# Performance work log

Measured on AMD Instinct MI355X. Metric: run time of the kernel, lower is better.

## Reference

```python
import math
import jax, jax.numpy as jnp
import numpy as np


def _expmap0(u):
    # geoopt Lorentz (k=1) expmap0 followed by projection back onto the hyperboloid.
    # Minkowski norm of the tangent input (geoopt clamps at 1e-8 before sqrt).
    u0 = u[..., :1]
    us = u[..., 1:]
    mink = -u0 * u0 + jnp.sum(us * us, axis=-1, keepdims=True)
    nomin = jnp.sqrt(jnp.maximum(mink, 1e-8))
    r = jnp.sinh(nomin) * u / nomin
    space = r[..., 1:]
    time = jnp.sqrt(1.0 + jnp.sum(space * space, axis=-1, keepdims=True))  # project()
    return jnp.concatenate([time, space], axis=-1)


def setup_inputs() -> dict:
    key = jax.random.key(0)
    B, T, E, H = 2, 1024, 1024, 16
    ks = jax.random.split(key, 8)
    s = 0.02
    return {
        "x": jax.random.normal(ks[0], (B, T, E), jnp.float32),
        "Wqkv": jax.random.normal(ks[1], (3 * E, E), jnp.float32) * s,
        "bqkv": jnp.zeros((3 * E,), jnp.float32),
        "Wout": jax.random.normal(ks[2], (E, E), jnp.float32) * s,
        "bout": jnp.zeros((E,), jnp.float32),
        "Wimp": jax.random.normal(ks[3], (1, E), jnp.float32) * s,
        "bimp": jnp.zeros((1,), jnp.float32),
        "Walpha": jax.random.normal(ks[4], (H, E), jnp.float32) * s,
        "balpha": jnp.zeros((H,), jnp.float32),
        "spike_threshold": jnp.asarray(0.5, jnp.float32),
        "log_k": jnp.full((H,), 0.54, jnp.float32),
        "qk_scale": jnp.asarray(0.1, jnp.float32),
    }


def reference(x, Wqkv, bqkv, Wout, bout, Wimp, bimp, Walpha, balpha,
              spike_threshold, log_k, qk_scale):
    B, T, C = x.shape
    H = log_k.shape[0]
    D = C // H

    importance = jax.nn.sigmoid(x @ Wimp.T + bimp)          # (B,T,1)
    # torch.tril on the (T,1) trailing dims keeps every element -> no-op mask.
    spikes = (importance > spike_threshold).astype(x.dtype)
    spike_mask = spikes.reshape(B, 1, T, 1)

    alpha = jax.nn.sigmoid(x @ Walpha.T + balpha)           # (B,T,H)
    alpha = jnp.transpose(alpha, (0, 2, 1))[..., None]      # (B,H,T,1)

    qkv = (x @ Wqkv.T + bqkv).reshape(B, T, 3, H, D)
    q = jnp.transpose(qkv[:, :, 0], (0, 2, 1, 3))           # (B,H,T,D)
    k = jnp.transpose(qkv[:, :, 1], (0, 2, 1, 3))
    v = jnp.transpose(qkv[:, :, 2], (0, 2, 1, 3))

    scores_euclid = jnp.einsum('bhtd,bhsd->bhts', q, k) / math.sqrt(D)

    safe_scale = jax.nn.sigmoid(qk_scale) * 1.5
    qn = q / jnp.maximum(jnp.linalg.norm(q, axis=-1, keepdims=True), 1e-12) * safe_scale
    kn = k / jnp.maximum(jnp.linalg.norm(k, axis=-1, keepdims=True), 1e-12) * safe_scale
    q_hyp = _expmap0(qn)
    k_hyp = _expmap0(kn)

    inner = (-jnp.einsum('bhti,bhsi->bhts', q_hyp[..., :1], k_hyp[..., :1])
             + jnp.einsum('bhtd,bhsd->bhts', q_hyp[..., 1:], k_hyp[..., 1:]))
    curv_k = (jax.nn.softplus(log_k) + 1e-6).reshape(1, H, 1, 1)
    mdot = jnp.maximum(-inner, 1.0 + 1e-6)
    dist = jnp.arccosh(mdot)
    scores_hyper = -(dist * dist) / curv_k

    scores = (1.0 - alpha) * scores_euclid + alpha * scores_hyper
    causal = jnp.tril(jnp.ones((T, T), bool))
    scores = jnp.where(causal[None, None], scores, -jnp.inf)

    attn = jax.nn.softmax(scores, axis=-1) * spike_mask     # dropout disabled (eval)
    y = jnp.einsum('bhts,bhsd->bhtd', attn, v)
    y = jnp.transpose(y, (0, 2, 1, 3)).reshape(B, T, C)
    return y @ Wout.T + bout
```

## Files before the change

### kernel.cpp

```cpp
#include <hip/hip_runtime.h>
#include <math.h>

#define B_ 2
#define T_ 1024
#define E_ 1024
#define H_ 16
#define D_ 64
#define M_ (B_*T_)

typedef __bf16 bf16x8 __attribute__((ext_vector_type(8)));
typedef __bf16 bf16x4 __attribute__((ext_vector_type(4)));
typedef float f32x4 __attribute__((ext_vector_type(4)));

__device__ __forceinline__ void* ldsp(__bf16* base, int row, int byte) {
  return (char*)base + row * 128 + (byte ^ ((row & 7) << 4));
}

__device__ __forceinline__ void gload_lds16(const void* g, void* l) {
  __builtin_amdgcn_global_load_lds((const __attribute__((address_space(1))) void*)g,
                                   (__attribute__((address_space(3))) void*)l, 16, 0, 0);
}

#define XV4 524288
#define WQV4 786432
#define WOV4 262144
#define TOTV4 (XV4 + WQV4 + WOV4)
__global__ __launch_bounds__(256) void conv_kernel(
    const float* __restrict__ x, const float* __restrict__ Wqkv,
    const float* __restrict__ Wout,
    __bf16* __restrict__ xb, __bf16* __restrict__ Wqkvb, __bf16* __restrict__ Woutb) {
  for (size_t i = (size_t)blockIdx.x * blockDim.x + threadIdx.x; i < TOTV4;
       i += (size_t)gridDim.x * blockDim.x) {
    const float4* src; __bf16* dst; size_t off;
    if (i < XV4)            { src = (const float4*)x;    dst = xb;    off = i; }
    else if (i < XV4+WQV4)  { src = (const float4*)Wqkv; dst = Wqkvb; off = i - XV4; }
    else                    { src = (const float4*)Wout; dst = Woutb; off = i - XV4 - WQV4; }
    float4 val = src[off];
    bf16x4 o = {(__bf16)val.x, (__bf16)val.y, (__bf16)val.z, (__bf16)val.w};
    *(bf16x4*)(dst + off * 4) = o;
  }
}

__global__ __launch_bounds__(256) void imp_alpha_kernel(
    const float* __restrict__ x,
    const float* __restrict__ Wimp, const float* __restrict__ bimp,
    const float* __restrict__ Walpha, const float* __restrict__ balpha,
    const float* __restrict__ thr_p,
    float* __restrict__ spike, float* __restrict__ alpha) {
  int m = blockIdx.x;
  int tid = threadIdx.x;
  const float* xr = x + (size_t)m * E_;
  float part[17];
#pragma unroll
  for (int i = 0; i < 17; ++i) part[i] = 0.f;
  for (int e = tid; e < E_; e += 256) {
    float xv = xr[e];
    part[16] += xv * Wimp[e];
#pragma unroll
    for (int h = 0; h < 16; ++h) part[h] += xv * Walpha[h * E_ + e];
  }
  __shared__ float red[17][4];
  int lane = tid & 63, wv = tid >> 6;
#pragma unroll
  for (int i = 0; i < 17; ++i) {
    float v = part[i];
    for (int off = 32; off > 0; off >>= 1) v += __shfl_down(v, off, 64);
    if (lane == 0) red[i][wv] = v;
  }
  __syncthreads();
  if (tid < 17) {
    float v = red[tid][0] + red[tid][1] + red[tid][2] + red[tid][3];
    if (tid == 16) {
      float z = v + bimp[0];
      float sig = 1.f / (1.f + expf(-z));
      spike[m] = (sig > thr_p[0]) ? 1.f : 0.f;
    } else {
      float z = v + balpha[tid];
      float a = 1.f / (1.f + expf(-z));
      int b = m >> 10, t = m & (T_ - 1);
      alpha[((size_t)(b * H_ + tid)) * T_ + t] = a;
    }
  }
}

__global__ __launch_bounds__(256) void qkv_gemm_kernel(
    const __bf16* __restrict__ A, const __bf16* __restrict__ Bm,
    const float* __restrict__ bias,
    __bf16* __restrict__ q, __bf16* __restrict__ k, __bf16* __restrict__ v) {
  __shared__ __bf16 As[128 * 32];
  __shared__ __bf16 Bs[128 * 32];
  const int K = E_;
  int tid = threadIdx.x;
  int w = tid >> 6, lane = tid & 63, lr = lane & 15, g = lane >> 4;
  int m0 = blockIdx.y * 128, n0 = blockIdx.x * 128;
  int wr = (w >> 1) * 64, wc = (w & 1) * 64;

  int task0 = tid, task1 = tid + 256;
  int r0s = task0 >> 2, c0s = task0 & 3;
  int r1s = task1 >> 2, c1s = task1 & 3;
  const __bf16* gA0 = A + (size_t)(m0 + r0s) * K + c0s * 8;
  const __bf16* gA1 = A + (size_t)(m0 + r1s) * K + c1s * 8;
  const __bf16* gB0 = Bm + (size_t)(n0 + r0s) * K + c0s * 8;
  const __bf16* gB1 = Bm + (size_t)(n0 + r1s) * K + c1s * 8;
  __bf16* lA0 = As + task0 * 8;
  __bf16* lA1 = As + task1 * 8;
  __bf16* lB0 = Bs + task0 * 8;
  __bf16* lB1 = Bs + task1 * 8;

  f32x4 acc[4][4];
#pragma unroll
  for (int i = 0; i < 4; ++i)
#pragma unroll
    for (int j = 0; j < 4; ++j) acc[i][j] = (f32x4){0.f, 0.f, 0.f, 0.f};

  for (int k0 = 0; k0 < K; k0 += 32) {
    gload_lds16(gA0, lA0); gload_lds16(gA1, lA1);
    gload_lds16(gB0, lB0); gload_lds16(gB1, lB1);
    gA0 += 32; gA1 += 32; gB0 += 32; gB1 += 32;
    __syncthreads();
    bf16x8 af[4], bf[4];
#pragma unroll
    for (int i = 0; i < 4; ++i) af[i] = *(bf16x8*)&As[(wr + i * 16 + lr) * 32 + g * 8];
#pragma unroll
    for (int j = 0; j < 4; ++j) bf[j] = *(bf16x8*)&Bs[(wc + j * 16 + lr) * 32 + g * 8];
#pragma unroll
    for (int i = 0; i < 4; ++i)
#pragma unroll
      for (int j = 0; j < 4; ++j)
        acc[i][j] = __builtin_amdgcn_mfma_f32_16x16x32_bf16(af[i], bf[j], acc[i][j], 0, 0, 0);
    __syncthreads();
  }

#pragma unroll
  for (int i = 0; i < 4; ++i) {
#pragma unroll
    for (int r = 0; r < 4; ++r) {
      int m = m0 + wr + i * 16 + g * 4 + r;
      int b = m >> 10, t = m & (T_ - 1);
#pragma unroll
      for (int j = 0; j < 4; ++j) {
        int n = n0 + wc + j * 16 + lr;
        float val = acc[i][j][r] + bias[n];
        int comp = n >> 10, h = (n >> 6) & 15, d = n & 63;
        __bf16* dst = (comp == 0) ? q : ((comp == 1) ? k : v);
        dst[(((size_t)(b * H_ + h)) * T_ + t) * 64 + d] = (__bf16)val;
      }
    }
  }
}

__global__ __launch_bounds__(256) void hyp_kernel(
    const __bf16* __restrict__ q, const __bf16* __restrict__ k,
    const float* __restrict__ qk_scale_p,
    __bf16* __restrict__ qh, __bf16* __restrict__ khn) {
  int wid = blockIdx.x * 4 + (threadIdx.x >> 6);
  int lane = threadIdx.x & 63;
  int is_k = wid >> 15;
  int row = wid & 32767;
  const __bf16* src = (is_k ? k : q) + (size_t)row * 64;
  float u = (float)src[lane];
  float nsq = u * u;
#pragma unroll
  for (int off = 32; off > 0; off >>= 1) nsq += __shfl_xor(nsq, off, 64);
  float norm = fmaxf(sqrtf(nsq), 1e-12f);
  float ss = 1.5f / (1.f + expf(-qk_scale_p[0]));
  float un = u / norm * ss;
  float s2 = un * un;
  float tot = s2;
#pragma unroll
  for (int off = 32; off > 0; off >>= 1) tot += __shfl_xor(tot, off, 64);
  float un0 = __shfl(un, 0, 64);
  float mink = tot - 2.f * un0 * un0;
  float nomin = sqrtf(fmaxf(mink, 1e-8f));
  float sc = sinhf(nomin) / nomin;
  float r = sc * un;
  float sp2 = (lane == 0) ? 0.f : r * r;
  float sps = sp2;
#pragma unroll
  for (int off = 32; off > 0; off >>= 1) sps += __shfl_xor(sps, off, 64);
  float tm = sqrtf(1.f + sps);
  float outv = (lane == 0) ? tm : r;
  if (is_k && lane != 0) outv = -outv;
  (is_k ? khn : qh)[(size_t)row * 64 + lane] = (__bf16)outv;
}

__global__ __launch_bounds__(256) void attn_kernel(
    const __bf16* __restrict__ q, const __bf16* __restrict__ k, const __bf16* __restrict__ v,
    const __bf16* __restrict__ qh, const __bf16* __restrict__ khn,
    const float* __restrict__ alpha, const float* __restrict__ spike,
    const float* __restrict__ log_k, __bf16* __restrict__ y) {
  __shared__ __bf16 q_s[64 * 64];
  __shared__ __bf16 qh_s[64 * 64];
  __shared__ __bf16 k_s[64 * 64];
  __shared__ __bf16 kh_s[64 * 64];
  __shared__ __bf16 vt_s[64 * 64];
  __shared__ __bf16 p_s[64 * 64];

  int bid = blockIdx.x;
  int bq = bid >> 5;
  int qi = (bq < 8) ? (15 - bq) : (bq - 8);
  int bh = bid & 31;
  int b = bh >> 4, h = bh & 15;
  int t0 = qi * 64;
  int tid = threadIdx.x;
  int w = tid >> 6, lane = tid & 63;
  int lr = lane & 15, g = lane >> 4;
  int trow = w * 16;
  const size_t base = (size_t)bh * T_ * 64;

#pragma unroll
  for (int it = 0; it < 2; ++it) {
    int task = tid + it * 256;
    int row = task >> 3, cj = task & 7;
    bf16x8 a = *(const bf16x8*)(q + base + (size_t)(t0 + row) * 64 + cj * 8);
    bf16x8 c = *(const bf16x8*)(qh + base + (size_t)(t0 + row) * 64 + cj * 8);
    *(bf16x8*)ldsp(q_s, row, cj * 16) = a;
    *(bf16x8*)ldsp(qh_s, row, cj * 16) = c;
  }

  float curv = log1pf(expf(log_k[h])) + 1e-6f;
  float hc = 0.69314718056f / curv;
  const float ec = 0.18033688f;
  int tg[4];
  float al[4], spv[4];
#pragma unroll
  for (int r = 0; r < 4; ++r) {
    tg[r] = t0 + trow + g * 4 + r;
    al[r] = alpha[(size_t)bh * T_ + tg[r]];
    spv[r] = spike[(size_t)b * T_ + tg[r]];
  }

  __syncthreads();
  bf16x8 aq0 = *(bf16x8*)ldsp(q_s, trow + lr, g * 16);
  bf16x8 aq1 = *(bf16x8*)ldsp(q_s, trow + lr, 64 + g * 16);
  bf16x8 ah0 = *(bf16x8*)ldsp(qh_s, trow + lr, g * 16);
  bf16x8 ah1 = *(bf16x8*)ldsp(qh_s, trow + lr, 64 + g * 16);

  float m_r[4] = {-1e30f, -1e30f, -1e30f, -1e30f};
  float l_r[4] = {0.f, 0.f, 0.f, 0.f};
  f32x4 acc[4];
#pragma unroll
  for (int n = 0; n < 4; ++n) acc[n] = (f32x4){0.f, 0.f, 0.f, 0.f};

  for (int st = 0; st <= qi; ++st) {
    int s0 = st * 64;
    bool diag = (st == qi);
    __syncthreads();
#pragma unroll
    for (int it = 0; it < 2; ++it) {
      int task = tid + it * 256;
      int row = task >> 3, cj = task & 7;
      bf16x8 a = *(const bf16x8*)(k + base + (size_t)(s0 + row) * 64 + cj * 8);
      bf16x8 c = *(const bf16x8*)(khn + base + (size_t)(s0 + row) * 64 + cj * 8);
      *(bf16x8*)ldsp(k_s, row, cj * 16) = a;
      *(bf16x8*)ldsp(kh_s, row, cj * 16) = c;
    }
#pragma unroll
    for (int it = 0; it < 2; ++it) {
      int task = tid + it * 256;
      int srow = task & 63, dc = task >> 6;
      bf16x8 a = *(const bf16x8*)(v + base + (size_t)(s0 + srow) * 64 + dc * 8);
#pragma unroll
      for (int i = 0; i < 8; ++i)
        *(__bf16*)ldsp(vt_s, dc * 8 + i, srow * 2) = a[i];
    }
    __syncthreads();

    float pv[4][4];
    float pmax[4] = {-1e30f, -1e30f, -1e30f, -1e30f};
#pragma unroll
    for (int j = 0; j < 4; ++j) {
      if (diag && (s0 + j * 16 > t0 + trow + 15)) {
#pragma unroll
        for (int r = 0; r < 4; ++r) pv[j][r] = -1e30f;
        continue;
      }
      bf16x8 bk0 = *(bf16x8*)ldsp(k_s, j * 16 + lr, g * 16);
      bf16x8 bk1 = *(bf16x8*)ldsp(k_s, j * 16 + lr, 64 + g * 16);
      f32x4 z = {0.f, 0.f, 0.f, 0.f};
      z = __builtin_amdgcn_mfma_f32_16x16x32_bf16(aq0, bk0, z, 0, 0, 0);
      f32x4 se = __builtin_amdgcn_mfma_f32_16x16x32_bf16(aq1, bk1, z, 0, 0, 0);
      bf16x8 bh0 = *(bf16x8*)ldsp(kh_s, j * 16 + lr, g * 16);
      bf16x8 bh1 = *(bf16x8*)ldsp(kh_s, j * 16 + lr, 64 + g * 16);
      f32x4 z2 = {0.f, 0.f, 0.f, 0.f};
      z2 = __builtin_amdgcn_mfma_f32_16x16x32_bf16(ah0, bh0, z2, 0, 0, 0);
      f32x4 sh = __builtin_amdgcn_mfma_f32_16x16x32_bf16(ah1, bh1, z2, 0, 0, 0);
      int sg = s0 + j * 16 + lr;
#pragma unroll
      for (int r = 0; r < 4; ++r) {
        float sc_e = se[r] * ec;
        float md = fmaxf(sh[r], 1.0f + 1e-6f);
        float l2 = __log2f(md + sqrtf(fmaf(md, md, -1.f)));
        float t = fmaf(l2 * l2, hc, sc_e);
        float s = fmaf(-al[r], t, sc_e);
        if (diag && sg > tg[r]) s = -1e30f;
        pv[j][r] = s;
        pmax[r] = fmaxf(pmax[r], s);
      }
    }
#pragma unroll
    for (int r = 0; r < 4; ++r) {
      float mx = pmax[r];
      mx = fmaxf(mx, __shfl_xor(mx, 1, 64));
      mx = fmaxf(mx, __shfl_xor(mx, 2, 64));
      mx = fmaxf(mx, __shfl_xor(mx, 4, 64));
      mx = fmaxf(mx, __shfl_xor(mx, 8, 64));
      float mn = fmaxf(m_r[r], mx);
      float fac = exp2f(m_r[r] - mn);
      m_r[r] = mn;
      float ls = 0.f;
#pragma unroll
      for (int j = 0; j < 4; ++j) { pv[j][r] = exp2f(pv[j][r] - mn); ls += pv[j][r]; }
      ls += __shfl_xor(ls, 1, 64);
      ls += __shfl_xor(ls, 2, 64);
      ls += __shfl_xor(ls, 4, 64);
      ls += __shfl_xor(ls, 8, 64);
      l_r[r] = l_r[r] * fac + ls;
#pragma unroll
      for (int n = 0; n < 4; ++n) acc[n][r] *= fac;
    }
#pragma unroll
    for (int j = 0; j < 4; ++j)
#pragma unroll
      for (int r = 0; r < 4; ++r)
        *(__bf16*)ldsp(p_s, trow + g * 4 + r, (j * 16 + lr) * 2) = (__bf16)pv[j][r];
    __syncthreads();

    bf16x8 ap0 = *(bf16x8*)ldsp(p_s, trow + lr, g * 16);
    bf16x8 ap1 = *(bf16x8*)ldsp(p_s, trow + lr, 64 + g * 16);
#pragma unroll
    for (int n = 0; n < 4; ++n) {
      bf16x8 bv0 = *(bf16x8*)ldsp(vt_s, n * 16 + lr, g * 16);
      bf16x8 bv1 = *(bf16x8*)ldsp(vt_s, n * 16 + lr, 64 + g * 16);
      acc[n] = __builtin_amdgcn_mfma_f32_16x16x32_bf16(ap0, bv0, acc[n], 0, 0, 0);
      acc[n] = __builtin_amdgcn_mfma_f32_16x16x32_bf16(ap1, bv1, acc[n], 0, 0, 0);
    }
  }

#pragma unroll
  for (int r = 0; r < 4; ++r) {
    float iv = spv[r] / l_r[r];
#pragma unroll
    for (int n = 0; n < 4; ++n) {
      y[((size_t)(b * T_ + tg[r])) * E_ + h * 64 + n * 16 + lr] =
          (__bf16)(acc[n][r] * iv);
    }
  }
}

__global__ __launch_bounds__(256) void out_gemm_kernel(
    const __bf16* __restrict__ A, const __bf16* __restrict__ Bm,
    const float* __restrict__ bias, float* __restrict__ outp) {
  __shared__ __bf16 As[128 * 32];
  __shared__ __bf16 Bs[128 * 32];
  const int K = E_;
  int tid = threadIdx.x;
  int w = tid >> 6, lane = tid & 63, lr = lane & 15, g = lane >> 4;
  int m0 = blockIdx.y * 128, n0 = blockIdx.x * 128;
  int wr = (w >> 1) * 64, wc = (w & 1) * 64;

  int task0 = tid, task1 = tid + 256;
  int r0s = task0 >> 2, c0s = task0 & 3;
  int r1s = task1 >> 2, c1s = task1 & 3;
  const __bf16* gA0 = A + (size_t)(m0 + r0s) * K + c0s * 8;
  const __bf16* gA1 = A + (size_t)(m0 + r1s) * K + c1s * 8;
  const __bf16* gB0 = Bm + (size_t)(n0 + r0s) * K + c0s * 8;
  const __bf16* gB1 = Bm + (size_t)(n0 + r1s) * K + c1s * 8;
  __bf16* lA0 = As + task0 * 8;
  __bf16* lA1 = As + task1 * 8;
  __bf16* lB0 = Bs + task0 * 8;
  __bf16* lB1 = Bs + task1 * 8;

  f32x4 acc[4][4];
#pragma unroll
  for (int i = 0; i < 4; ++i)
#pragma unroll
    for (int j = 0; j < 4; ++j) acc[i][j] = (f32x4){0.f, 0.f, 0.f, 0.f};

  for (int k0 = 0; k0 < K; k0 += 32) {
    gload_lds16(gA0, lA0); gload_lds16(gA1, lA1);
    gload_lds16(gB0, lB0); gload_lds16(gB1, lB1);
    gA0 += 32; gA1 += 32; gB0 += 32; gB1 += 32;
    __syncthreads();
    bf16x8 af[4], bf[4];
#pragma unroll
    for (int i = 0; i < 4; ++i) af[i] = *(bf16x8*)&As[(wr + i * 16 + lr) * 32 + g * 8];
#pragma unroll
    for (int j = 0; j < 4; ++j) bf[j] = *(bf16x8*)&Bs[(wc + j * 16 + lr) * 32 + g * 8];
#pragma unroll
    for (int i = 0; i < 4; ++i)
#pragma unroll
      for (int j = 0; j < 4; ++j)
        acc[i][j] = __builtin_amdgcn_mfma_f32_16x16x32_bf16(af[i], bf[j], acc[i][j], 0, 0, 0);
    __syncthreads();
  }

#pragma unroll
  for (int i = 0; i < 4; ++i) {
#pragma unroll
    for (int r = 0; r < 4; ++r) {
      int m = m0 + wr + i * 16 + g * 4 + r;
#pragma unroll
      for (int j = 0; j < 4; ++j) {
        int n = n0 + wc + j * 16 + lr;
        outp[(size_t)m * E_ + n] = acc[i][j][r] + bias[n];
      }
    }
  }
}

extern "C" void kernel_launch(void* const* d_in, const int* in_sizes, int n_in,
                              void* d_out, int out_size, void* d_ws, size_t ws_size,
                              hipStream_t stream) {
  const float* x      = (const float*)d_in[0];
  const float* Wqkv   = (const float*)d_in[1];
  const float* bqkv   = (const float*)d_in[2];
  const float* Wout   = (const float*)d_in[3];
  const float* bout   = (const float*)d_in[4];
  const float* Wimp   = (const float*)d_in[5];
  const float* bimp   = (const float*)d_in[6];
  const float* Walpha = (const float*)d_in[7];
  const float* balpha = (const float*)d_in[8];
  const float* thr    = (const float*)d_in[9];
  const float* log_k  = (const float*)d_in[10];
  const float* qk_sc  = (const float*)d_in[11];
  float* out = (float*)d_out;

  char* ws = (char*)d_ws;
  size_t off = 0;
  auto alloc = [&](size_t bytes) -> void* {
    void* p = (void*)(ws + off);
    off += (bytes + 255) & ~(size_t)255;
    return p;
  };
  const size_t qkv_elems = (size_t)B_ * H_ * T_ * D_;
  __bf16* xb    = (__bf16*)alloc((size_t)M_ * E_ * 2);
  __bf16* Wqkvb = (__bf16*)alloc((size_t)3 * E_ * E_ * 2);
  __bf16* Woutb = (__bf16*)alloc((size_t)E_ * E_ * 2);
  __bf16* q   = (__bf16*)alloc(qkv_elems * 2);
  __bf16* k   = (__bf16*)alloc(qkv_elems * 2);
  __bf16* v   = (__bf16*)alloc(qkv_elems * 2);
  __bf16* qh  = (__bf16*)alloc(qkv_elems * 2);
  __bf16* khn = (__bf16*)alloc(qkv_elems * 2);
  __bf16* yw  = (__bf16*)alloc((size_t)M_ * E_ * 2);
  float* alphaw = (float*)alloc((size_t)B_ * H_ * T_ * sizeof(float));
  float* spikew = (float*)alloc((size_t)M_ * sizeof(float));

  conv_kernel<<<1024, 256, 0, stream>>>(x, Wqkv, Wout, xb, Wqkvb, Woutb);
  imp_alpha_kernel<<<M_, 256, 0, stream>>>(x, Wimp, bimp, Walpha, balpha, thr,
                                           spikew, alphaw);
  qkv_gemm_kernel<<<dim3(24, 16), 256, 0, stream>>>(xb, Wqkvb, bqkv, q, k, v);
  hyp_kernel<<<(2 * B_ * H_ * T_) / 4, 256, 0, stream>>>(q, k, qk_sc, qh, khn);
  attn_kernel<<<B_ * H_ * (T_ / 64), 256, 0, stream>>>(q, k, v, qh, khn,
                                                       alphaw, spikew, log_k, yw);
  out_gemm_kernel<<<dim3(8, 16), 256, 0, stream>>>(yw, Woutb, bout, out);
}
```

Baseline: 157.9 us.

## Split attention into per-wave query tiles with split-KV partials and merge

Attention now gives each wave its own 16-row query tile and processes alternate key tiles (two halves), writing unnormalised partial accumulators plus running max and sum. A new merge kernel combines the two halves and applies the spike mask and normalisation. V is pre-transposed once by a new kernel so PV operands load straight from global memory, and block-wide LDS staging and barriers are dropped. The aim is better load balance and more parallelism under the causal mask, and less synchronisation. The cost is that K, KH and V are no longer shared through LDS across waves, so L2 traffic rises, and the two extra launches add partial-buffer traffic.

```diff
diff --git a/kernel.cpp b/kernel.cpp
--- a/kernel.cpp
+++ b/kernel.cpp
@@ -184,57 +184,69 @@
   (is_k ? khn : qh)[(size_t)row * 64 + lane] = (__bf16)outv;
 }
 
-__global__ __launch_bounds__(256) void attn_kernel(
-    const __bf16* __restrict__ q, const __bf16* __restrict__ k, const __bf16* __restrict__ v,
-    const __bf16* __restrict__ qh, const __bf16* __restrict__ khn,
-    const float* __restrict__ alpha, const float* __restrict__ spike,
-    const float* __restrict__ log_k, __bf16* __restrict__ y) {
-  __shared__ __bf16 q_s[64 * 64];
-  __shared__ __bf16 qh_s[64 * 64];
-  __shared__ __bf16 k_s[64 * 64];
-  __shared__ __bf16 kh_s[64 * 64];
-  __shared__ __bf16 vt_s[64 * 64];
-  __shared__ __bf16 p_s[64 * 64];
-
-  int bid = blockIdx.x;
-  int bq = bid >> 5;
-  int qi = (bq < 8) ? (15 - bq) : (bq - 8);
-  int bh = bid & 31;
-  int b = bh >> 4, h = bh & 15;
-  int t0 = qi * 64;
-  int tid = threadIdx.x;
-  int w = tid >> 6, lane = tid & 63;
-  int lr = lane & 15, g = lane >> 4;
-  int trow = w * 16;
-  const size_t base = (size_t)bh * T_ * 64;
-
+__global__ __launch_bounds__(256) void vtr_kernel(
+    const __bf16* __restrict__ v, __bf16* __restrict__ vt) {
+  __shared__ __bf16 tile[64][65];
+  int bh = blockIdx.x >> 4;
+  int s0 = (blockIdx.x & 15) * 64;
+  int tid = threadIdx.x;
 #pragma unroll
   for (int it = 0; it < 2; ++it) {
     int task = tid + it * 256;
-    int row = task >> 3, cj = task & 7;
-    bf16x8 a = *(const bf16x8*)(q + base + (size_t)(t0 + row) * 64 + cj * 8);
-    bf16x8 c = *(const bf16x8*)(qh + base + (size_t)(t0 + row) * 64 + cj * 8);
-    *(bf16x8*)ldsp(q_s, row, cj * 16) = a;
-    *(bf16x8*)ldsp(qh_s, row, cj * 16) = c;
-  }
+    int r = task >> 3, c = (task & 7) * 8;
+    bf16x8 a = *(const bf16x8*)(v + ((size_t)bh * T_ + s0 + r) * 64 + c);
+#pragma unroll
+    for (int i = 0; i < 8; ++i) tile[r][c + i] = a[i];
+  }
+  __syncthreads();
+#pragma unroll
+  for (int it = 0; it < 2; ++it) {
+    int task = tid + it * 256;
+    int dd = task >> 3, sc = (task & 7) * 8;
+    bf16x8 o;
+#pragma unroll
+    for (int i = 0; i < 8; ++i) o[i] = tile[sc + i][dd];
+    *(bf16x8*)(vt + ((size_t)bh * 64 + dd) * T_ + s0 + sc) = o;
+  }
+}
+
+__global__ __launch_bounds__(256) void attn_kernel(
+    const __bf16* __restrict__ q, const __bf16* __restrict__ k,
+    const __bf16* __restrict__ qh, const __bf16* __restrict__ khn,
+    const __bf16* __restrict__ vt,
+    const float* __restrict__ alpha, const float* __restrict__ log_k,
+    __bf16* __restrict__ pacc, float* __restrict__ pml) {
+  __shared__ __bf16 pslab_all[4][16 * 64];
+  int tid = threadIdx.x;
+  int w = tid >> 6, lane = tid & 63;
+  int wid = blockIdx.x * 4 + w;
+  int bh = wid & 31;
+  int rest = wid >> 5;
+  int half = rest & 1;
+  int qt = rest >> 1;
+  int h = bh & 15;
+  int lr = lane & 15, g = lane >> 4;
+  int n_st = (qt >> 2) + 1;
+  const size_t base = (size_t)bh * T_ * 64;
+  const size_t vtb = (size_t)bh * 64 * T_;
+  __bf16* pslab = pslab_all[w];
+
+  const __bf16* qrow = q + base + (size_t)(qt * 16 + lr) * 64;
+  const __bf16* qhrow = qh + base + (size_t)(qt * 16 + lr) * 64;
+  bf16x8 aq0 = *(const bf16x8*)(qrow + g * 8);
+  bf16x8 aq1 = *(const bf16x8*)(qrow + 32 + g * 8);
+  bf16x8 ah0 = *(const bf16x8*)(qhrow + g * 8);
+  bf16x8 ah1 = *(const bf16x8*)(qhrow + 32 + g * 8);
 
   float curv = log1pf(expf(log_k[h])) + 1e-6f;
   float hc = 0.69314718056f / curv;
   const float ec = 0.18033688f;
-  int tg[4];
-  float al[4], spv[4];
+  int tg[4]; float al[4];
 #pragma unroll
   for (int r = 0; r < 4; ++r) {
-    tg[r] = t0 + trow + g * 4 + r;
+    tg[r] = qt * 16 + g * 4 + r;
     al[r] = alpha[(size_t)bh * T_ + tg[r]];
-    spv[r] = spike[(size_t)b * T_ + tg[r]];
-  }
-
-  __syncthreads();
-  bf16x8 aq0 = *(bf16x8*)ldsp(q_s, trow + lr, g * 16);
-  bf16x8 aq1 = *(bf16x8*)ldsp(q_s, trow + lr, 64 + g * 16);
-  bf16x8 ah0 = *(bf16x8*)ldsp(qh_s, trow + lr, g * 16);
-  bf16x8 ah1 = *(bf16x8*)ldsp(qh_s, trow + lr, 64 + g * 16);
+  }
 
   float m_r[4] = {-1e30f, -1e30f, -1e30f, -1e30f};
   float l_r[4] = {0.f, 0.f, 0.f, 0.f};
@@ -242,46 +254,27 @@
 #pragma unroll
   for (int n = 0; n < 4; ++n) acc[n] = (f32x4){0.f, 0.f, 0.f, 0.f};
 
-  for (int st = 0; st <= qi; ++st) {
+  for (int st = half; st < n_st; st += 2) {
     int s0 = st * 64;
-    bool diag = (st == qi);
-    __syncthreads();
-#pragma unroll
-    for (int it = 0; it < 2; ++it) {
-      int task = tid + it * 256;
-      int row = task >> 3, cj = task & 7;
-      bf16x8 a = *(const bf16x8*)(k + base + (size_t)(s0 + row) * 64 + cj * 8);
-      bf16x8 c = *(const bf16x8*)(khn + base + (size_t)(s0 + row) * 64 + cj * 8);
-      *(bf16x8*)ldsp(k_s, row, cj * 16) = a;
-      *(bf16x8*)ldsp(kh_s, row, cj * 16) = c;
-    }
-#pragma unroll
-    for (int it = 0; it < 2; ++it) {
-      int task = tid + it * 256;
-      int srow = task & 63, dc = task >> 6;
-      bf16x8 a = *(const bf16x8*)(v + base + (size_t)(s0 + srow) * 64 + dc * 8);
-#pragma unroll
-      for (int i = 0; i < 8; ++i)
-        *(__bf16*)ldsp(vt_s, dc * 8 + i, srow * 2) = a[i];
-    }
-    __syncthreads();
-
+    bool diag = (st == n_st - 1);
     float pv[4][4];
     float pmax[4] = {-1e30f, -1e30f, -1e30f, -1e30f};
 #pragma unroll
     for (int j = 0; j < 4; ++j) {
-      if (diag && (s0 + j * 16 > t0 + trow + 15)) {
+      if (diag && (s0 + j * 16 > qt * 16 + 15)) {
 #pragma unroll
         for (int r = 0; r < 4; ++r) pv[j][r] = -1e30f;
         continue;
       }
-      bf16x8 bk0 = *(bf16x8*)ldsp(k_s, j * 16 + lr, g * 16);
-      bf16x8 bk1 = *(bf16x8*)ldsp(k_s, j * 16 + lr, 64 + g * 16);
+      const __bf16* kr = k + base + (size_t)(s0 + j * 16 + lr) * 64;
+      const __bf16* khr = khn + base + (size_t)(s0 + j * 16 + lr) * 64;
+      bf16x8 bk0 = *(const bf16x8*)(kr + g * 8);
+      bf16x8 bk1 = *(const bf16x8*)(kr + 32 + g * 8);
       f32x4 z = {0.f, 0.f, 0.f, 0.f};
       z = __builtin_amdgcn_mfma_f32_16x16x32_bf16(aq0, bk0, z, 0, 0, 0);
       f32x4 se = __builtin_amdgcn_mfma_f32_16x16x32_bf16(aq1, bk1, z, 0, 0, 0);
-      bf16x8 bh0 = *(bf16x8*)ldsp(kh_s, j * 16 + lr, g * 16);
-      bf16x8 bh1 = *(bf16x8*)ldsp(kh_s, j * 16 + lr, 64 + g * 16);
+      bf16x8 bh0 = *(const bf16x8*)(khr + g * 8);
+      bf16x8 bh1 = *(const bf16x8*)(khr + 32 + g * 8);
       f32x4 z2 = {0.f, 0.f, 0.f, 0.f};
       z2 = __builtin_amdgcn_mfma_f32_16x16x32_bf16(ah0, bh0, z2, 0, 0, 0);
       f32x4 sh = __builtin_amdgcn_mfma_f32_16x16x32_bf16(ah1, bh1, z2, 0, 0, 0);
@@ -323,28 +316,60 @@
     for (int j = 0; j < 4; ++j)
 #pragma unroll
       for (int r = 0; r < 4; ++r)
-        *(__bf16*)ldsp(p_s, trow + g * 4 + r, (j * 16 + lr) * 2) = (__bf16)pv[j][r];
-    __syncthreads();
-
-    bf16x8 ap0 = *(bf16x8*)ldsp(p_s, trow + lr, g * 16);
-    bf16x8 ap1 = *(bf16x8*)ldsp(p_s, trow + lr, 64 + g * 16);
+        *(__bf16*)ldsp(pslab, g * 4 + r, (j * 16 + lr) * 2) = (__bf16)pv[j][r];
+    bf16x8 ap0 = *(bf16x8*)ldsp(pslab, lr, g * 16);
+    bf16x8 ap1 = *(bf16x8*)ldsp(pslab, lr, 64 + g * 16);
 #pragma unroll
     for (int n = 0; n < 4; ++n) {
-      bf16x8 bv0 = *(bf16x8*)ldsp(vt_s, n * 16 + lr, g * 16);
-      bf16x8 bv1 = *(bf16x8*)ldsp(vt_s, n * 16 + lr, 64 + g * 16);
+      const __bf16* vr = vt + vtb + (size_t)(n * 16 + lr) * T_ + s0;
+      bf16x8 bv0 = *(const bf16x8*)(vr + g * 8);
+      bf16x8 bv1 = *(const bf16x8*)(vr + 32 + g * 8);
       acc[n] = __builtin_amdgcn_mfma_f32_16x16x32_bf16(ap0, bv0, acc[n], 0, 0, 0);
       acc[n] = __builtin_amdgcn_mfma_f32_16x16x32_bf16(ap1, bv1, acc[n], 0, 0, 0);
     }
   }
 
-#pragma unroll
-  for (int r = 0; r < 4; ++r) {
-    float iv = spv[r] / l_r[r];
-#pragma unroll
-    for (int n = 0; n < 4; ++n) {
-      y[((size_t)(b * T_ + tg[r])) * E_ + h * 64 + n * 16 + lr] =
-          (__bf16)(acc[n][r] * iv);
-    }
+  int pidx = ((bh << 6) + qt) * 2 + half;
+  __bf16* pa = pacc + (size_t)pidx * 1024;
+#pragma unroll
+  for (int n = 0; n < 4; ++n)
+#pragma unroll
+    for (int r = 0; r < 4; ++r)
+      pa[(g * 4 + r) * 64 + n * 16 + lr] = (__bf16)acc[n][r];
+  if (lr == 0) {
+#pragma unroll
+    for (int r = 0; r < 4; ++r) {
+      pml[(size_t)pidx * 32 + g * 4 + r] = m_r[r];
+      pml[(size_t)pidx * 32 + 16 + g * 4 + r] = l_r[r];
+    }
+  }
+}
+
+__global__ __launch_bounds__(256) void merge_kernel(
+    const __bf16* __restrict__ pacc, const float* __restrict__ pml,
+    const float* __restrict__ spike, __bf16* __restrict__ yw) {
+  int tid = threadIdx.x;
+  int w = tid >> 6, lane = tid & 63;
+  int wid = blockIdx.x * 4 + w;
+  int bh = wid & 31;
+  int qt = wid >> 5;
+  int b = bh >> 4, h = bh & 15;
+  size_t i1 = ((size_t)(bh << 6) + qt) * 2;
+  size_t i2 = i1 + 1;
+  const __bf16* a1 = pacc + i1 * 1024;
+  const __bf16* a2 = pacc + i2 * 1024;
+#pragma unroll 4
+  for (int row = 0; row < 16; ++row) {
+    float m1 = pml[i1 * 32 + row], l1 = pml[i1 * 32 + 16 + row];
+    float m2 = pml[i2 * 32 + row], l2 = pml[i2 * 32 + 16 + row];
+    float mm = fmaxf(m1, m2);
+    float f1 = exp2f(m1 - mm), f2 = exp2f(m2 - mm);
+    float l = l1 * f1 + l2 * f2;
+    int t = qt * 16 + row;
+    float iv = spike[(size_t)b * T_ + t] / l;
+    float val = ((float)a1[row * 64 + lane] * f1 +
+                 (float)a2[row * 64 + lane] * f2) * iv;
+    yw[(size_t)(b * T_ + t) * E_ + h * 64 + lane] = (__bf16)val;
   }
 }
 
@@ -442,16 +467,21 @@
   __bf16* v   = (__bf16*)alloc(qkv_elems * 2);
   __bf16* qh  = (__bf16*)alloc(qkv_elems * 2);
   __bf16* khn = (__bf16*)alloc(qkv_elems * 2);
+  __bf16* vt  = (__bf16*)alloc(qkv_elems * 2);
   __bf16* yw  = (__bf16*)alloc((size_t)M_ * E_ * 2);
   float* alphaw = (float*)alloc((size_t)B_ * H_ * T_ * sizeof(float));
   float* spikew = (float*)alloc((size_t)M_ * sizeof(float));
+  float* pml    = (float*)alloc((size_t)4096 * 32 * sizeof(float));
+  __bf16* pacc = (__bf16*)ws;
 
   conv_kernel<<<1024, 256, 0, stream>>>(x, Wqkv, Wout, xb, Wqkvb, Woutb);
   imp_alpha_kernel<<<M_, 256, 0, stream>>>(x, Wimp, bimp, Walpha, balpha, thr,
                                            spikew, alphaw);
   qkv_gemm_kernel<<<dim3(24, 16), 256, 0, stream>>>(xb, Wqkvb, bqkv, q, k, v);
   hyp_kernel<<<(2 * B_ * H_ * T_) / 4, 256, 0, stream>>>(q, k, qk_sc, qh, khn);
-  attn_kernel<<<B_ * H_ * (T_ / 64), 256, 0, stream>>>(q, k, v, qh, khn,
-                                                       alphaw, spikew, log_k, yw);
+  vtr_kernel<<<B_ * H_ * (T_ / 64), 256, 0, stream>>>(v, vt);
+  attn_kernel<<<1024, 256, 0, stream>>>(q, k, qh, khn, vt, alphaw, log_k,
+                                        pacc, pml);
+  merge_kernel<<<512, 256, 0, stream>>>(pacc, pml, spikew, yw);
   out_gemm_kernel<<<dim3(8, 16), 256, 0, stream>>>(yw, Woutb, bout, out);
 }
```

Result: slower. 183.4 us (+16.2%).
